# Performance work log

Measured on AMD Instinct MI355X. Metric: run time of the kernel, lower is better.

The kernel has to match this reference:

```python
import jax, jax.numpy as jnp
import numpy as np

G_DOWNSAMPLED = 16  # g_downsampled_dimension: tiling factor
XF_DIM = 1024       # xf_dimension
BATCH = 2048


def setup_inputs() -> dict:
    key = jax.random.key(0)
    k1, k2 = jax.random.split(key)
    xf = jax.random.normal(k1, (BATCH, XF_DIM), dtype=jnp.float32)
    wp = jax.random.normal(k2, (1,), dtype=jnp.float32)
    return {"xf": xf, "wp": wp}


def reference(xf, wp):
    # xf_r = relu(xf - mean_batch(xf))
    xf_r = jax.nn.relu(xf - jnp.mean(xf, axis=0))
    # fn_xf = (xf_r - mean(xf_r)) / std(xf_r), std unbiased (torch default ddof=1)
    mu = jnp.mean(xf_r, axis=0)
    sd = jnp.std(xf_r, axis=0, ddof=1)
    fn_xf = (xf_r - mu) / sd
    # matmul with W_tile = kron(ones(1,g), eye(xf_dim)) is an exact tile along features
    x_ = wp * jnp.tile(fn_xf, (1, G_DOWNSAMPLED))  # [batch, g*xf_dim]
    return x_
```

## Files before the change

kernel.cpp:

```cpp
#include <hip/hip_runtime.h>

#define BATCH 2048
#define FDIM  1024
#define GTILE 16
#define F4    (FDIM / 4)
#define CHUNKS 32
#define ROWS_PER_CHUNK (BATCH / CHUNKS)

#define OFF_P1   0
#define OFF_P2S  32768
#define OFF_P2Q  65536
#define OFF_MEAN 98304
#define OFF_SC   99328
#define OFF_CC   100352

__global__ void k1_partial_sum(const float4* __restrict__ xf, float4* __restrict__ p1) {
    const int tid = threadIdx.x;
    const int chunk = blockIdx.x;
    const float4* p = xf + (size_t)chunk * ROWS_PER_CHUNK * F4 + tid;
    float4 s = {0.f, 0.f, 0.f, 0.f};
#pragma unroll 8
    for (int r = 0; r < ROWS_PER_CHUNK; ++r) {
        float4 v = p[r * F4];
        s.x += v.x; s.y += v.y; s.z += v.z; s.w += v.w;
    }
    p1[chunk * F4 + tid] = s;
}

__global__ void k2_relu_partial(const float4* __restrict__ xf,
                                const float4* __restrict__ p1,
                                float4* __restrict__ p2s,
                                float4* __restrict__ p2q) {
    const int tid = threadIdx.x;
    const int chunk = blockIdx.x;
    float4 m = {0.f, 0.f, 0.f, 0.f};
#pragma unroll
    for (int c = 0; c < CHUNKS; ++c) {
        float4 v = p1[c * F4 + tid];
        m.x += v.x; m.y += v.y; m.z += v.z; m.w += v.w;
    }
    const float inv_n = 1.0f / (float)BATCH;
    m.x *= inv_n; m.y *= inv_n; m.z *= inv_n; m.w *= inv_n;

    const float4* p = xf + (size_t)chunk * ROWS_PER_CHUNK * F4 + tid;
    float4 s = {0.f, 0.f, 0.f, 0.f};
    float4 q = {0.f, 0.f, 0.f, 0.f};
#pragma unroll 8
    for (int r = 0; r < ROWS_PER_CHUNK; ++r) {
        float4 v = p[r * F4];
        float rx = fmaxf(v.x - m.x, 0.f);
        float ry = fmaxf(v.y - m.y, 0.f);
        float rz = fmaxf(v.z - m.z, 0.f);
        float rw = fmaxf(v.w - m.w, 0.f);
        s.x += rx; s.y += ry; s.z += rz; s.w += rw;
        q.x += rx * rx; q.y += ry * ry; q.z += rz * rz; q.w += rw * rw;
    }
    p2s[chunk * F4 + tid] = s;
    p2q[chunk * F4 + tid] = q;
}

__global__ void k3_finalize(const float* __restrict__ wp,
                            const float4* __restrict__ p1,
                            const float4* __restrict__ p2s,
                            const float4* __restrict__ p2q,
                            float4* __restrict__ mean,
                            float4* __restrict__ sc,
                            float4* __restrict__ cc) {
    const int tid = threadIdx.x;
    float4 m = {0.f,0.f,0.f,0.f}, s = {0.f,0.f,0.f,0.f}, q = {0.f,0.f,0.f,0.f};
#pragma unroll
    for (int c = 0; c < CHUNKS; ++c) {
        float4 a = p1[c * F4 + tid];
        float4 b = p2s[c * F4 + tid];
        float4 d = p2q[c * F4 + tid];
        m.x += a.x; m.y += a.y; m.z += a.z; m.w += a.w;
        s.x += b.x; s.y += b.y; s.z += b.z; s.w += b.w;
        q.x += d.x; q.y += d.y; q.z += d.z; q.w += d.w;
    }
    const float inv_n = 1.0f / (float)BATCH;
    const float w = wp[0];
    float4 mn, scale, cmb;
    {
        float mu, var;
        mn.x = m.x * inv_n;
        mu = s.x * inv_n; var = (q.x - s.x * mu) / (float)(BATCH - 1);
        scale.x = w * rsqrtf(var); cmb.x = mu * scale.x;
        mn.y = m.y * inv_n;
        mu = s.y * inv_n; var = (q.y - s.y * mu) / (float)(BATCH - 1);
        scale.y = w * rsqrtf(var); cmb.y = mu * scale.y;
        mn.z = m.z * inv_n;
        mu = s.z * inv_n; var = (q.z - s.z * mu) / (float)(BATCH - 1);
        scale.z = w * rsqrtf(var); cmb.z = mu * scale.z;
        mn.w = m.w * inv_n;
        mu = s.w * inv_n; var = (q.w - s.w * mu) / (float)(BATCH - 1);
        scale.w = w * rsqrtf(var); cmb.w = mu * scale.w;
    }
    mean[tid] = mn;
    sc[tid]   = scale;
    cc[tid]   = cmb;
}

__global__ void k4_write(const float4* __restrict__ xf,
                         const float4* __restrict__ mean,
                         const float4* __restrict__ sc,
                         const float4* __restrict__ cc,
                         float4* __restrict__ out) {
    const int tid = threadIdx.x;
    const int row = blockIdx.x;
    float4 m = mean[tid];
    float4 a = sc[tid];
    float4 c = cc[tid];
    float4 v = xf[(size_t)row * F4 + tid];
    float4 o;
    o.x = fmaxf(v.x - m.x, 0.f) * a.x - c.x;
    o.y = fmaxf(v.y - m.y, 0.f) * a.y - c.y;
    o.z = fmaxf(v.z - m.z, 0.f) * a.z - c.z;
    o.w = fmaxf(v.w - m.w, 0.f) * a.w - c.w;
    float4* dst = out + (size_t)row * (GTILE * F4) + tid;
#pragma unroll
    for (int g = 0; g < GTILE; ++g) {
        dst[g * F4] = o;
    }
}

extern "C" void kernel_launch(void* const* d_in, const int* in_sizes, int n_in,
                              void* d_out, int out_size, void* d_ws, size_t ws_size,
                              hipStream_t stream) {
    const float* xf = (const float*)d_in[0];
    const float* wp = (const float*)d_in[1];
    float* ws = (float*)d_ws;
    float* out = (float*)d_out;

    const float4* xf4 = (const float4*)xf;
    float4* p1  = (float4*)(ws + OFF_P1);
    float4* p2s = (float4*)(ws + OFF_P2S);
    float4* p2q = (float4*)(ws + OFF_P2Q);
    float4* mean = (float4*)(ws + OFF_MEAN);
    float4* sc   = (float4*)(ws + OFF_SC);
    float4* cc   = (float4*)(ws + OFF_CC);

    k1_partial_sum<<<CHUNKS, 256, 0, stream>>>(xf4, p1);
    k2_relu_partial<<<CHUNKS, 256, 0, stream>>>(xf4, p1, p2s, p2q);
    k3_finalize<<<1, 256, 0, stream>>>(wp, p1, p2s, p2q, mean, sc, cc);
    k4_write<<<BATCH, 256, 0, stream>>>(xf4, mean, sc, cc, (float4*)out);
}
```

Baseline: 159.5 us.

## Widen reduction chunks, parallelize finalize, and use nontemporal output stores

Raises the number of reduction chunks from 32 to 128 so the two statistics passes launch more blocks and spread the read of xf over more compute units. The finalize kernel now runs 1024 threads, splits the chunk partials four ways, and combines them through shared memory. The output-tiling kernel writes with nontemporal stores so the large replicated output does not pollute the cache. The cost is more partial-sum traffic in the workspace and an extra shared-memory reduction step.

After: 176.0 us. 1.1x slower.

```diff
diff --git a/kernel.cpp b/kernel.cpp
--- a/kernel.cpp
+++ b/kernel.cpp
@@ -4,22 +4,24 @@
 #define FDIM  1024
 #define GTILE 16
 #define F4    (FDIM / 4)
-#define CHUNKS 32
+#define CHUNKS 128
 #define ROWS_PER_CHUNK (BATCH / CHUNKS)
 
+typedef float nvec4 __attribute__((ext_vector_type(4)));
+
 #define OFF_P1   0
-#define OFF_P2S  32768
-#define OFF_P2Q  65536
-#define OFF_MEAN 98304
-#define OFF_SC   99328
-#define OFF_CC   100352
+#define OFF_P2S  131072
+#define OFF_P2Q  262144
+#define OFF_MEAN 393216
+#define OFF_SC   394240
+#define OFF_CC   395264
 
 __global__ void k1_partial_sum(const float4* __restrict__ xf, float4* __restrict__ p1) {
     const int tid = threadIdx.x;
     const int chunk = blockIdx.x;
     const float4* p = xf + (size_t)chunk * ROWS_PER_CHUNK * F4 + tid;
     float4 s = {0.f, 0.f, 0.f, 0.f};
-#pragma unroll 8
+#pragma unroll
     for (int r = 0; r < ROWS_PER_CHUNK; ++r) {
         float4 v = p[r * F4];
         s.x += v.x; s.y += v.y; s.z += v.z; s.w += v.w;
@@ -34,7 +36,7 @@
     const int tid = threadIdx.x;
     const int chunk = blockIdx.x;
     float4 m = {0.f, 0.f, 0.f, 0.f};
-#pragma unroll
+#pragma unroll 8
     for (int c = 0; c < CHUNKS; ++c) {
         float4 v = p1[c * F4 + tid];
         m.x += v.x; m.y += v.y; m.z += v.z; m.w += v.w;
@@ -45,7 +47,7 @@
     const float4* p = xf + (size_t)chunk * ROWS_PER_CHUNK * F4 + tid;
     float4 s = {0.f, 0.f, 0.f, 0.f};
     float4 q = {0.f, 0.f, 0.f, 0.f};
-#pragma unroll 8
+#pragma unroll
     for (int r = 0; r < ROWS_PER_CHUNK; ++r) {
         float4 v = p[r * F4];
         float rx = fmaxf(v.x - m.x, 0.f);
@@ -66,60 +68,78 @@
                             float4* __restrict__ mean,
                             float4* __restrict__ sc,
                             float4* __restrict__ cc) {
+    __shared__ float4 red[3 * 4 * F4];
     const int tid = threadIdx.x;
+    const int cg = tid & (F4 - 1);
+    const int part = tid >> 8;
     float4 m = {0.f,0.f,0.f,0.f}, s = {0.f,0.f,0.f,0.f}, q = {0.f,0.f,0.f,0.f};
-#pragma unroll
-    for (int c = 0; c < CHUNKS; ++c) {
-        float4 a = p1[c * F4 + tid];
-        float4 b = p2s[c * F4 + tid];
-        float4 d = p2q[c * F4 + tid];
+    const int c0 = part * (CHUNKS / 4);
+#pragma unroll 8
+    for (int c = c0; c < c0 + CHUNKS / 4; ++c) {
+        float4 a = p1[c * F4 + cg];
+        float4 b = p2s[c * F4 + cg];
+        float4 d = p2q[c * F4 + cg];
         m.x += a.x; m.y += a.y; m.z += a.z; m.w += a.w;
         s.x += b.x; s.y += b.y; s.z += b.z; s.w += b.w;
         q.x += d.x; q.y += d.y; q.z += d.z; q.w += d.w;
     }
-    const float inv_n = 1.0f / (float)BATCH;
-    const float w = wp[0];
-    float4 mn, scale, cmb;
-    {
+    red[(0 * 4 + part) * F4 + cg] = m;
+    red[(1 * 4 + part) * F4 + cg] = s;
+    red[(2 * 4 + part) * F4 + cg] = q;
+    __syncthreads();
+    if (tid < F4) {
+        float4 M = {0.f,0.f,0.f,0.f}, S = {0.f,0.f,0.f,0.f}, Q = {0.f,0.f,0.f,0.f};
+#pragma unroll
+        for (int p = 0; p < 4; ++p) {
+            float4 a = red[(0 * 4 + p) * F4 + tid];
+            float4 b = red[(1 * 4 + p) * F4 + tid];
+            float4 d = red[(2 * 4 + p) * F4 + tid];
+            M.x += a.x; M.y += a.y; M.z += a.z; M.w += a.w;
+            S.x += b.x; S.y += b.y; S.z += b.z; S.w += b.w;
+            Q.x += d.x; Q.y += d.y; Q.z += d.z; Q.w += d.w;
+        }
+        const float inv_n = 1.0f / (float)BATCH;
+        const float w = wp[0];
+        float4 mn, scale, cmb;
         float mu, var;
-        mn.x = m.x * inv_n;
-        mu = s.x * inv_n; var = (q.x - s.x * mu) / (float)(BATCH - 1);
+        mn.x = M.x * inv_n;
+        mu = S.x * inv_n; var = (Q.x - S.x * mu) / (float)(BATCH - 1);
         scale.x = w * rsqrtf(var); cmb.x = mu * scale.x;
-        mn.y = m.y * inv_n;
-        mu = s.y * inv_n; var = (q.y - s.y * mu) / (float)(BATCH - 1);
+        mn.y = M.y * inv_n;
+        mu = S.y * inv_n; var = (Q.y - S.y * mu) / (float)(BATCH - 1);
         scale.y = w * rsqrtf(var); cmb.y = mu * scale.y;
-        mn.z = m.z * inv_n;
-        mu = s.z * inv_n; var = (q.z - s.z * mu) / (float)(BATCH - 1);
+        mn.z = M.z * inv_n;
+        mu = S.z * inv_n; var = (Q.z - S.z * mu) / (float)(BATCH - 1);
         scale.z = w * rsqrtf(var); cmb.z = mu * scale.z;
-        mn.w = m.w * inv_n;
-        mu = s.w * inv_n; var = (q.w - s.w * mu) / (float)(BATCH - 1);
+        mn.w = M.w * inv_n;
+        mu = S.w * inv_n; var = (Q.w - S.w * mu) / (float)(BATCH - 1);
         scale.w = w * rsqrtf(var); cmb.w = mu * scale.w;
+        mean[tid] = mn;
+        sc[tid]   = scale;
+        cc[tid]   = cmb;
     }
-    mean[tid] = mn;
-    sc[tid]   = scale;
-    cc[tid]   = cmb;
 }
 
 __global__ void k4_write(const float4* __restrict__ xf,
                          const float4* __restrict__ mean,
                          const float4* __restrict__ sc,
                          const float4* __restrict__ cc,
-                         float4* __restrict__ out) {
+                         float* __restrict__ out) {
     const int tid = threadIdx.x;
     const int row = blockIdx.x;
     float4 m = mean[tid];
     float4 a = sc[tid];
     float4 c = cc[tid];
     float4 v = xf[(size_t)row * F4 + tid];
-    float4 o;
+    nvec4 o;
     o.x = fmaxf(v.x - m.x, 0.f) * a.x - c.x;
     o.y = fmaxf(v.y - m.y, 0.f) * a.y - c.y;
     o.z = fmaxf(v.z - m.z, 0.f) * a.z - c.z;
     o.w = fmaxf(v.w - m.w, 0.f) * a.w - c.w;
-    float4* dst = out + (size_t)row * (GTILE * F4) + tid;
+    nvec4* dst = (nvec4*)(out + (size_t)row * (GTILE * FDIM)) + tid;
 #pragma unroll
     for (int g = 0; g < GTILE; ++g) {
-        dst[g * F4] = o;
+        __builtin_nontemporal_store(o, &dst[g * F4]);
     }
 }
 
@@ -141,6 +161,6 @@
 
     k1_partial_sum<<<CHUNKS, 256, 0, stream>>>(xf4, p1);
     k2_relu_partial<<<CHUNKS, 256, 0, stream>>>(xf4, p1, p2s, p2q);
-    k3_finalize<<<1, 256, 0, stream>>>(wp, p1, p2s, p2q, mean, sc, cc);
-    k4_write<<<BATCH, 256, 0, stream>>>(xf4, mean, sc, cc, (float4*)out);
+    k3_finalize<<<1, 1024, 0, stream>>>(wp, p1, p2s, p2q, mean, sc, cc);
+    k4_write<<<BATCH, 256, 0, stream>>>(xf4, mean, sc, cc, out);
 }
```

## Fuse stats kernels into one cooperative kernel with wider grid and grid syncs

Applied to the files above, without the earlier changes.

Replaces the three statistics kernels, which used only 32 blocks, with a single cooperative kernel of 256 blocks. Grid-wide syncs separate the phases, and the cross-block reductions run in shared memory with each block owning one feature group. The aim is to use more of the GPU for the two passes over the input and to remove separate launch overhead. In exchange it adds three grid.sync barriers and a cooperative launch, and the workspace grows to hold 256 partials per feature.

After: 240.5 us. +50.8%, slower.

```diff
diff --git a/kernel.cpp b/kernel.cpp
--- a/kernel.cpp
+++ b/kernel.cpp
@@ -1,103 +1,111 @@
 #include <hip/hip_runtime.h>
+#include <hip/hip_cooperative_groups.h>
+
+namespace cg = cooperative_groups;
 
 #define BATCH 2048
 #define FDIM  1024
 #define GTILE 16
 #define F4    (FDIM / 4)
-#define CHUNKS 32
-#define ROWS_PER_CHUNK (BATCH / CHUNKS)
+#define NBLK  256
+#define ROWS  (BATCH / NBLK)
 
 #define OFF_P1   0
-#define OFF_P2S  32768
-#define OFF_P2Q  65536
-#define OFF_MEAN 98304
-#define OFF_SC   99328
-#define OFF_CC   100352
+#define OFF_P2S  262144
+#define OFF_P2Q  524288
+#define OFF_MEAN 786432
+#define OFF_SC   787456
+#define OFF_CC   788480
 
-__global__ void k1_partial_sum(const float4* __restrict__ xf, float4* __restrict__ p1) {
-    const int tid = threadIdx.x;
-    const int chunk = blockIdx.x;
-    const float4* p = xf + (size_t)chunk * ROWS_PER_CHUNK * F4 + tid;
-    float4 s = {0.f, 0.f, 0.f, 0.f};
-#pragma unroll 8
-    for (int r = 0; r < ROWS_PER_CHUNK; ++r) {
-        float4 v = p[r * F4];
-        s.x += v.x; s.y += v.y; s.z += v.z; s.w += v.w;
-    }
-    p1[chunk * F4 + tid] = s;
+__device__ __forceinline__ void v4add(float4& a, const float4& b) {
+    a.x += b.x; a.y += b.y; a.z += b.z; a.w += b.w;
 }
 
-__global__ void k2_relu_partial(const float4* __restrict__ xf,
-                                const float4* __restrict__ p1,
-                                float4* __restrict__ p2s,
-                                float4* __restrict__ p2q) {
+__global__ void __launch_bounds__(256) kstats(const float4* __restrict__ xf,
+                                              const float* __restrict__ wp,
+                                              float4* __restrict__ p1,
+                                              float4* __restrict__ p2s,
+                                              float4* __restrict__ p2q,
+                                              float4* __restrict__ mean,
+                                              float4* __restrict__ sc,
+                                              float4* __restrict__ cc) {
+    cg::grid_group grid = cg::this_grid();
     const int tid = threadIdx.x;
-    const int chunk = blockIdx.x;
-    float4 m = {0.f, 0.f, 0.f, 0.f};
+    const int b   = blockIdx.x;
+    __shared__ float4 redA[256];
+    __shared__ float4 redB[256];
+
+    {
+        const float4* p = xf + (size_t)b * ROWS * F4 + tid;
+        float4 s = {0.f, 0.f, 0.f, 0.f};
 #pragma unroll
-    for (int c = 0; c < CHUNKS; ++c) {
-        float4 v = p1[c * F4 + tid];
-        m.x += v.x; m.y += v.y; m.z += v.z; m.w += v.w;
+        for (int r = 0; r < ROWS; ++r) v4add(s, p[r * F4]);
+        p1[b * F4 + tid] = s;
     }
-    const float inv_n = 1.0f / (float)BATCH;
-    m.x *= inv_n; m.y *= inv_n; m.z *= inv_n; m.w *= inv_n;
+    grid.sync();
 
-    const float4* p = xf + (size_t)chunk * ROWS_PER_CHUNK * F4 + tid;
-    float4 s = {0.f, 0.f, 0.f, 0.f};
-    float4 q = {0.f, 0.f, 0.f, 0.f};
-#pragma unroll 8
-    for (int r = 0; r < ROWS_PER_CHUNK; ++r) {
-        float4 v = p[r * F4];
-        float rx = fmaxf(v.x - m.x, 0.f);
-        float ry = fmaxf(v.y - m.y, 0.f);
-        float rz = fmaxf(v.z - m.z, 0.f);
-        float rw = fmaxf(v.w - m.w, 0.f);
-        s.x += rx; s.y += ry; s.z += rz; s.w += rw;
-        q.x += rx * rx; q.y += ry * ry; q.z += rz * rz; q.w += rw * rw;
+    {
+        redA[tid] = p1[tid * F4 + b];
+        __syncthreads();
+        for (int off = 128; off > 0; off >>= 1) {
+            if (tid < off) v4add(redA[tid], redA[tid + off]);
+            __syncthreads();
+        }
+        if (tid == 0) {
+            const float inv_n = 1.0f / (float)BATCH;
+            float4 m = redA[0];
+            m.x *= inv_n; m.y *= inv_n; m.z *= inv_n; m.w *= inv_n;
+            mean[b] = m;
+        }
     }
-    p2s[chunk * F4 + tid] = s;
-    p2q[chunk * F4 + tid] = q;
-}
+    grid.sync();
 
-__global__ void k3_finalize(const float* __restrict__ wp,
-                            const float4* __restrict__ p1,
-                            const float4* __restrict__ p2s,
-                            const float4* __restrict__ p2q,
-                            float4* __restrict__ mean,
-                            float4* __restrict__ sc,
-                            float4* __restrict__ cc) {
-    const int tid = threadIdx.x;
-    float4 m = {0.f,0.f,0.f,0.f}, s = {0.f,0.f,0.f,0.f}, q = {0.f,0.f,0.f,0.f};
+    {
+        float4 m = mean[tid];
+        const float4* p = xf + (size_t)b * ROWS * F4 + tid;
+        float4 s = {0.f, 0.f, 0.f, 0.f};
+        float4 q = {0.f, 0.f, 0.f, 0.f};
 #pragma unroll
-    for (int c = 0; c < CHUNKS; ++c) {
-        float4 a = p1[c * F4 + tid];
-        float4 b = p2s[c * F4 + tid];
-        float4 d = p2q[c * F4 + tid];
-        m.x += a.x; m.y += a.y; m.z += a.z; m.w += a.w;
-        s.x += b.x; s.y += b.y; s.z += b.z; s.w += b.w;
-        q.x += d.x; q.y += d.y; q.z += d.z; q.w += d.w;
+        for (int r = 0; r < ROWS; ++r) {
+            float4 v = p[r * F4];
+            float rx = fmaxf(v.x - m.x, 0.f);
+            float ry = fmaxf(v.y - m.y, 0.f);
+            float rz = fmaxf(v.z - m.z, 0.f);
+            float rw = fmaxf(v.w - m.w, 0.f);
+            s.x += rx; s.y += ry; s.z += rz; s.w += rw;
+            q.x += rx * rx; q.y += ry * ry; q.z += rz * rz; q.w += rw * rw;
+        }
+        p2s[b * F4 + tid] = s;
+        p2q[b * F4 + tid] = q;
     }
-    const float inv_n = 1.0f / (float)BATCH;
-    const float w = wp[0];
-    float4 mn, scale, cmb;
+    grid.sync();
+
     {
-        float mu, var;
-        mn.x = m.x * inv_n;
-        mu = s.x * inv_n; var = (q.x - s.x * mu) / (float)(BATCH - 1);
-        scale.x = w * rsqrtf(var); cmb.x = mu * scale.x;
-        mn.y = m.y * inv_n;
-        mu = s.y * inv_n; var = (q.y - s.y * mu) / (float)(BATCH - 1);
-        scale.y = w * rsqrtf(var); cmb.y = mu * scale.y;
-        mn.z = m.z * inv_n;
-        mu = s.z * inv_n; var = (q.z - s.z * mu) / (float)(BATCH - 1);
-        scale.z = w * rsqrtf(var); cmb.z = mu * scale.z;
-        mn.w = m.w * inv_n;
-        mu = s.w * inv_n; var = (q.w - s.w * mu) / (float)(BATCH - 1);
-        scale.w = w * rsqrtf(var); cmb.w = mu * scale.w;
+        redA[tid] = p2s[tid * F4 + b];
+        redB[tid] = p2q[tid * F4 + b];
+        __syncthreads();
+        for (int off = 128; off > 0; off >>= 1) {
+            if (tid < off) { v4add(redA[tid], redA[tid + off]); v4add(redB[tid], redB[tid + off]); }
+            __syncthreads();
+        }
+        if (tid == 0) {
+            const float inv_n = 1.0f / (float)BATCH;
+            const float w = wp[0];
+            float4 S = redA[0], Q = redB[0];
+            float4 scale, cmb;
+            float mu, var;
+            mu = S.x * inv_n; var = (Q.x - S.x * mu) / (float)(BATCH - 1);
+            scale.x = w * rsqrtf(var); cmb.x = mu * scale.x;
+            mu = S.y * inv_n; var = (Q.y - S.y * mu) / (float)(BATCH - 1);
+            scale.y = w * rsqrtf(var); cmb.y = mu * scale.y;
+            mu = S.z * inv_n; var = (Q.z - S.z * mu) / (float)(BATCH - 1);
+            scale.z = w * rsqrtf(var); cmb.z = mu * scale.z;
+            mu = S.w * inv_n; var = (Q.w - S.w * mu) / (float)(BATCH - 1);
+            scale.w = w * rsqrtf(var); cmb.w = mu * scale.w;
+            sc[b] = scale;
+            cc[b] = cmb;
+        }
     }
-    mean[tid] = mn;
-    sc[tid]   = scale;
-    cc[tid]   = cmb;
 }
 
 __global__ void k4_write(const float4* __restrict__ xf,
@@ -126,21 +134,21 @@
 extern "C" void kernel_launch(void* const* d_in, const int* in_sizes, int n_in,
                               void* d_out, int out_size, void* d_ws, size_t ws_size,
                               hipStream_t stream) {
-    const float* xf = (const float*)d_in[0];
+    const float4* xf4 = (const float4*)d_in[0];
     const float* wp = (const float*)d_in[1];
     float* ws = (float*)d_ws;
-    float* out = (float*)d_out;
+    float4* out = (float4*)d_out;
 
-    const float4* xf4 = (const float4*)xf;
-    float4* p1  = (float4*)(ws + OFF_P1);
-    float4* p2s = (float4*)(ws + OFF_P2S);
-    float4* p2q = (float4*)(ws + OFF_P2Q);
+    float4* p1   = (float4*)(ws + OFF_P1);
+    float4* p2s  = (float4*)(ws + OFF_P2S);
+    float4* p2q  = (float4*)(ws + OFF_P2Q);
     float4* mean = (float4*)(ws + OFF_MEAN);
     float4* sc   = (float4*)(ws + OFF_SC);
     float4* cc   = (float4*)(ws + OFF_CC);
 
-    k1_partial_sum<<<CHUNKS, 256, 0, stream>>>(xf4, p1);
-    k2_relu_partial<<<CHUNKS, 256, 0, stream>>>(xf4, p1, p2s, p2q);
-    k3_finalize<<<1, 256, 0, stream>>>(wp, p1, p2s, p2q, mean, sc, cc);
-    k4_write<<<BATCH, 256, 0, stream>>>(xf4, mean, sc, cc, (float4*)out);
+    void* args[] = { (void*)&xf4, (void*)&wp, (void*)&p1, (void*)&p2s,
+                     (void*)&p2q, (void*)&mean, (void*)&sc, (void*)&cc };
+    hipLaunchCooperativeKernel((const void*)kstats, dim3(NBLK), dim3(256),
+                               args, 0, stream);
+    k4_write<<<BATCH, 256, 0, stream>>>(xf4, mean, sc, cc, out);
 }
```
